# Kernel optimization log

Measured on AMD Instinct MI355X. Metric: run time of the kernel, lower is better.

The kernel has to match this reference:

```python
import jax, jax.numpy as jnp
import numpy as np

N = 100000      # num nodes
E = 1600000     # num edges (avg degree 16)
ND = 32         # node_dim
ED = 32         # edge_dim
OD = 32         # out_dim


def setup_inputs() -> dict:
    key = jax.random.key(0)
    ks = jax.random.split(key, 7)
    node_x = jax.random.normal(ks[0], (N, ND), dtype=jnp.float32)
    edge_x = jax.random.normal(ks[1], (E, ED), dtype=jnp.float32)
    # forward() initializes g.ndata['z'] = torch.rand(N, node_dim+edge_dim)
    z_init = jax.random.uniform(ks[2], (N, ND + ED), dtype=jnp.float32)
    # pre_layer: Linear(ND+ED -> ND+ED); update_layer: Linear(2*ND+ED -> OD)
    W_pre = jax.random.normal(ks[3], (ND + ED, ND + ED), dtype=jnp.float32) / np.sqrt(ND + ED)
    b_pre = jnp.zeros((ND + ED,), dtype=jnp.float32)
    W_upd = jax.random.normal(ks[4], (2 * ND + ED, OD), dtype=jnp.float32) / np.sqrt(2 * ND + ED)
    b_upd = jnp.zeros((OD,), dtype=jnp.float32)
    src = jax.random.randint(ks[5], (E,), 0, N, dtype=jnp.int32)
    dst = jax.random.randint(ks[6], (E,), 0, N, dtype=jnp.int32)
    return {"node_x": node_x, "edge_x": edge_x, "z_init": z_init,
            "W_pre": W_pre, "b_pre": b_pre, "W_upd": W_upd, "b_upd": b_upd,
            "src": src, "dst": dst}


def reference(node_x, edge_x, z_init, W_pre, b_pre, W_upd, b_upd, src, dst):
    n = node_x.shape[0]
    # msg_func: per-edge gather + concat + Linear. Messages depend only on the
    # STATIC node feature 'x', so DGL's topological propagation is equivalent
    # to one edge-parallel pass.
    msg = jnp.concatenate([node_x[src], edge_x], axis=1) @ W_pre + b_pre  # [E, ND+ED]
    # reduce_func: sum over mailbox + ReLU (only fires for nodes with in-edges;
    # nodes with no incoming edges keep the random z_init).
    agg = jax.ops.segment_sum(msg, dst, num_segments=n)                    # [N, ND+ED]
    deg = jax.ops.segment_sum(jnp.ones_like(dst, dtype=node_x.dtype), dst, num_segments=n)
    z = jnp.where((deg > 0)[:, None], jax.nn.relu(agg), z_init)           # [N, ND+ED]
    # node_update: concat + Linear + ReLU
    h = jax.nn.relu(jnp.concatenate([node_x, z], axis=1) @ W_upd + b_upd)  # [N, OD]
    return h
```

## Files before the change

### kernel.cpp

```cpp
#include <hip/hip_runtime.h>


#define N_NODES 100000
#define N_EDGES 1600000
#define ND 32
#define ED 32
#define OD 32
#define ZD 64
#define NTILE 98
#define SLOTS 128
#define NWAVE (N_EDGES / SLOTS + 1)

__device__ inline float bcast(float v, int lane) {
    return __uint_as_float(__builtin_amdgcn_readlane(__float_as_uint(v), lane));
}

__global__ __launch_bounds__(256) void hist8(const int* __restrict__ dst,
                                             int* __restrict__ h8) {
    int e = blockIdx.x * 256 + threadIdx.x;
    if (e < N_EDGES)
        atomicAdd(&h8[(blockIdx.x & 7) * N_NODES + dst[e]], 1);
}

__global__ __launch_bounds__(1024) void scan_part(const int* __restrict__ h8,
                                                  int* __restrict__ cnt,
                                                  int* __restrict__ part) {
    __shared__ int s[1024];
    int i = blockIdx.x * 1024 + threadIdx.x;
    int v = 0;
    if (i < N_NODES) {
        #pragma unroll
        for (int x = 0; x < 8; ++x) v += h8[x * N_NODES + i];
        cnt[i] = v;
    }
    s[threadIdx.x] = v;
    __syncthreads();
    for (int off = 512; off > 0; off >>= 1) {
        if (threadIdx.x < off) s[threadIdx.x] += s[threadIdx.x + off];
        __syncthreads();
    }
    if (threadIdx.x == 0) part[blockIdx.x] = s[0];
}

__global__ void scan_top(int* part) {
    __shared__ int s[128];
    int v = (threadIdx.x < NTILE) ? part[threadIdx.x] : 0;
    s[threadIdx.x] = v;
    __syncthreads();
    for (int off = 1; off < 128; off <<= 1) {
        int u = (threadIdx.x >= off) ? s[threadIdx.x - off] : 0;
        __syncthreads();
        s[threadIdx.x] += u;
        __syncthreads();
    }
    if (threadIdx.x < NTILE) part[threadIdx.x] = s[threadIdx.x] - v;
}

__global__ __launch_bounds__(1024) void scan_local(const int* __restrict__ cnt,
                                                   const int* __restrict__ part,
                                                   const int* __restrict__ h8,
                                                   int* __restrict__ cursor,
                                                   int* __restrict__ c8) {
    __shared__ int s[1024];
    int i = blockIdx.x * 1024 + threadIdx.x;
    int v = (i < N_NODES) ? cnt[i] : 0;
    s[threadIdx.x] = v;
    __syncthreads();
    for (int off = 1; off < 1024; off <<= 1) {
        int u = (threadIdx.x >= off) ? s[threadIdx.x - off] : 0;
        __syncthreads();
        s[threadIdx.x] += u;
        __syncthreads();
    }
    if (i < N_NODES) {
        int run = part[blockIdx.x] + s[threadIdx.x] - v;
        cursor[i] = run;
        #pragma unroll
        for (int x = 0; x < 8; ++x) {
            c8[x * N_NODES + i] = run;
            run += h8[x * N_NODES + i];
        }
    }
}

__global__ __launch_bounds__(256) void permute_ids(
    const int* __restrict__ src, const int* __restrict__ dst,
    int* __restrict__ c8, int2* __restrict__ pair)
{
    int e = blockIdx.x * 256 + threadIdx.x;
    if (e >= N_EDGES) return;
    int pos = atomicAdd(&c8[(blockIdx.x & 7) * N_NODES + dst[e]], 1);
    pair[pos] = make_int2(src[e], e);
}

__device__ inline int lbound(const int* __restrict__ cur, int x) {
    int lo = 0, hi = N_NODES;
    while (lo < hi) {
        int mid = (lo + hi) >> 1;
        if (cur[mid] < x) lo = mid + 1; else hi = mid;
    }
    return lo;
}

__global__ __launch_bounds__(256, 1) void z_csr(
    const float* __restrict__ node_x, const float* __restrict__ edge_x,
    const float* __restrict__ z_init,
    const float* __restrict__ W_pre, const float* __restrict__ b_pre,
    const int* __restrict__ cursor,
    const int2* __restrict__ pair, float* __restrict__ zbuf)
{
    const int l = threadIdx.x & 63;
    float Wp[ZD];
    #pragma unroll
    for (int k = 0; k < ZD; ++k) Wp[k] = W_pre[k * ZD + l];
    const float bp = b_pre[l];
    const float* __restrict__ gbase = (l < ND) ? node_x : (edge_x - ND);

    int w = ((blockIdx.x * 256 + threadIdx.x) >> 6);
    if (w >= NWAVE) return;
    int lo = w * SLOTS;
    int n0 = lbound(cursor, lo);
    int n1 = lbound(cursor, lo + SLOTS);

    for (int n = n0; n < n1; ++n) {
        int j   = cursor[n];
        int end = (n + 1 < N_NODES) ? cursor[n + 1] : N_EDGES;
        int dg  = end - j;
        float z;
        if (dg > 0) {
            float acc = 0.0f;
            for (; j + 8 <= end; j += 8) {
                int2 p0 = pair[j],   p1 = pair[j+1], p2 = pair[j+2], p3 = pair[j+3];
                int2 p4 = pair[j+4], p5 = pair[j+5], p6 = pair[j+6], p7 = pair[j+7];
                int s0 = (l < ND) ? p0.x : p0.y;
                int s1 = (l < ND) ? p1.x : p1.y;
                int s2 = (l < ND) ? p2.x : p2.y;
                int s3 = (l < ND) ? p3.x : p3.y;
                int s4 = (l < ND) ? p4.x : p4.y;
                int s5 = (l < ND) ? p5.x : p5.y;
                int s6 = (l < ND) ? p6.x : p6.y;
                int s7 = (l < ND) ? p7.x : p7.y;
                float v0 = gbase[(unsigned)s0 * 32u + (unsigned)l];
                float v1 = gbase[(unsigned)s1 * 32u + (unsigned)l];
                float v2 = gbase[(unsigned)s2 * 32u + (unsigned)l];
                float v3 = gbase[(unsigned)s3 * 32u + (unsigned)l];
                float v4 = gbase[(unsigned)s4 * 32u + (unsigned)l];
                float v5 = gbase[(unsigned)s5 * 32u + (unsigned)l];
                float v6 = gbase[(unsigned)s6 * 32u + (unsigned)l];
                float v7 = gbase[(unsigned)s7 * 32u + (unsigned)l];
                acc += ((v0 + v1) + (v2 + v3)) + ((v4 + v5) + (v6 + v7));
            }
            for (; j < end; ++j) {
                int2 p0 = pair[j];
                int s0 = (l < ND) ? p0.x : p0.y;
                acc += gbase[(unsigned)s0 * 32u + (unsigned)l];
            }
            float a0 = (float)dg * bp, a1 = 0.0f;
            #pragma unroll
            for (int k = 0; k < ZD; k += 2) {
                a0 += bcast(acc, k)     * Wp[k];
                a1 += bcast(acc, k + 1) * Wp[k + 1];
            }
            z = fmaxf(a0 + a1, 0.0f);
        } else {
            z = z_init[(long)n * ZD + l];
        }
        zbuf[(long)n * ZD + l] = z;
    }
}

__global__ __launch_bounds__(256) void edge_scatter(
    const float* __restrict__ node_x, const float* __restrict__ edge_x,
    const int* __restrict__ src, const int* __restrict__ dst,
    float* __restrict__ S, int* __restrict__ degI)
{
    long t = (long)blockIdx.x * 256 + threadIdx.x;
    int e = (int)(t >> 6), l = (int)(t & 63);
    if (e >= N_EDGES) return;
    int s = src[e], d = dst[e];
    float v = (l < ND) ? node_x[(long)s * ND + l] : edge_x[(long)e * ED + (l - ND)];
    atomicAdd(&S[(long)d * ZD + l], v);
    if (l == 0) atomicAdd(&degI[d], 1);
}

__global__ __launch_bounds__(256, 1) void z_dense(
    const float* __restrict__ z_init,
    const float* __restrict__ W_pre, const float* __restrict__ b_pre,
    float* __restrict__ S, const int* __restrict__ degI)
{
    const int l = threadIdx.x & 63;
    float Wp[ZD];
    #pragma unroll
    for (int k = 0; k < ZD; ++k) Wp[k] = W_pre[k * ZD + l];
    const float bp = b_pre[l];
    int w  = (blockIdx.x * 256 + threadIdx.x) >> 6;
    int nw = (gridDim.x * 256) >> 6;
    for (int n = w; n < N_NODES; n += nw) {
        int dg = degI[n];
        float sv = S[(long)n * ZD + l];
        float z;
        if (dg > 0) {
            float a0 = (float)dg * bp, a1 = 0.0f;
            #pragma unroll
            for (int k = 0; k < ZD; k += 2) {
                a0 += bcast(sv, k)     * Wp[k];
                a1 += bcast(sv, k + 1) * Wp[k + 1];
            }
            z = fmaxf(a0 + a1, 0.0f);
        } else {
            z = z_init[(long)n * ZD + l];
        }
        S[(long)n * ZD + l] = z;
    }
}

__global__ __launch_bounds__(256, 1) void h_upd(
    const float* __restrict__ node_x,
    const float* __restrict__ W_upd, const float* __restrict__ b_upd,
    const float* __restrict__ zbuf, float* __restrict__ out)
{
    const int l = threadIdx.x & 63;
    const int c = l & 31;
    float Wu[ND + ZD];
    #pragma unroll
    for (int k = 0; k < ND + ZD; ++k) Wu[k] = W_upd[k * OD + c];
    const float bu = b_upd[c];
    int w  = (blockIdx.x * 256 + threadIdx.x) >> 6;
    int nw = (gridDim.x * 256) >> 6;
    for (int n = w; n < N_NODES; n += nw) {
        float zv = zbuf[(long)n * ZD + l];
        float xv = node_x[(long)n * ND + c];
        float h0 = bu, h1 = 0.0f;
        #pragma unroll
        for (int k = 0; k < ND; k += 2) {
            h0 += bcast(xv, k)     * Wu[k];
            h1 += bcast(xv, k + 1) * Wu[k + 1];
        }
        #pragma unroll
        for (int k = 0; k < ZD; k += 2) {
            h0 += bcast(zv, k)     * Wu[ND + k];
            h1 += bcast(zv, k + 1) * Wu[ND + k + 1];
        }
        if (l < OD) out[(long)n * OD + l] = fmaxf(h0 + h1, 0.0f);
    }
}

extern "C" void kernel_launch(void* const* d_in, const int* in_sizes, int n_in,
                              void* d_out, int out_size, void* d_ws, size_t ws_size,
                              hipStream_t stream)
{
    const float* node_x = (const float*)d_in[0];
    const float* edge_x = (const float*)d_in[1];
    const float* z_init = (const float*)d_in[2];
    const float* W_pre  = (const float*)d_in[3];
    const float* b_pre  = (const float*)d_in[4];
    const float* W_upd  = (const float*)d_in[5];
    const float* b_upd  = (const float*)d_in[6];
    const int*   src    = (const int*)d_in[7];
    const int*   dst    = (const int*)d_in[8];
    float* out = (float*)d_out;

    size_t need = (size_t)N_EDGES * sizeof(int2)
                + (size_t)N_NODES * ZD * sizeof(float)
                + ((size_t)18 * N_NODES + 128) * sizeof(int);

    if (ws_size >= need) {
        int2*  pair   = (int2*)d_ws;
        float* zbuf   = (float*)(pair + N_EDGES);
        int*   cnt    = (int*)(zbuf + (size_t)N_NODES * ZD);
        int*   part   = cnt + N_NODES;
        int*   cursor = part + 128;
        int*   h8     = cursor + N_NODES;
        int*   c8     = h8 + 8 * N_NODES;

        (void)hipMemsetAsync(h8, 0, 8 * N_NODES * sizeof(int), stream);
        hist8<<<(N_EDGES + 255) / 256, 256, 0, stream>>>(dst, h8);
        scan_part<<<NTILE, 1024, 0, stream>>>(h8, cnt, part);
        scan_top<<<1, 128, 0, stream>>>(part);
        scan_local<<<NTILE, 1024, 0, stream>>>(cnt, part, h8, cursor, c8);
        permute_ids<<<(N_EDGES + 255) / 256, 256, 0, stream>>>(src, dst, c8, pair);
        z_csr<<<(NWAVE * 64 + 255) / 256, 256, 0, stream>>>(
            node_x, edge_x, z_init, W_pre, b_pre, cursor, pair, zbuf);
        h_upd<<<2048, 256, 0, stream>>>(node_x, W_upd, b_upd, zbuf, out);
    } else {
        float* S    = (float*)d_ws;
        int*   degI = (int*)(S + (size_t)N_NODES * ZD);
        (void)hipMemsetAsync(d_ws, 0,
            ((size_t)N_NODES * ZD + N_NODES) * sizeof(float), stream);
        edge_scatter<<<(int)(((long)N_EDGES * 64 + 255) / 256), 256, 0, stream>>>(
            node_x, edge_x, src, dst, S, degI);
        z_dense<<<2048, 256, 0, stream>>>(z_init, W_pre, b_pre, S, degI);
        h_upd<<<2048, 256, 0, stream>>>(node_x, W_upd, b_upd, S, out);
    }
}
```

Baseline: 721.5 us.

## Gather four edges per wave iteration with float4 loads in z_csr

Rewrites the CSR aggregation so each wave handles four edges at once: 16-lane groups each load one edge's 32 node features and 32 edge features as float4, then the groups are reduced with xor shuffles before the readlane-based matvec. Work is also redistributed from equal edge-slot chunks found by binary search to a grid-stride loop of one node per wave, with degree read from cnt. This is meant to cut per-edge load instructions and latency chains, but tail edges are handled with clamped masked loads, and load balance now depends on node degree.

```diff
diff --git a/kernel.cpp b/kernel.cpp
--- a/kernel.cpp
+++ b/kernel.cpp
@@ -8,8 +8,6 @@
 #define OD 32
 #define ZD 64
 #define NTILE 98
-#define SLOTS 128
-#define NWAVE (N_EDGES / SLOTS + 1)
 
 __device__ inline float bcast(float v, int lane) {
     return __uint_as_float(__builtin_amdgcn_readlane(__float_as_uint(v), lane));
@@ -93,73 +91,67 @@
     pair[pos] = make_int2(src[e], e);
 }
 
-__device__ inline int lbound(const int* __restrict__ cur, int x) {
-    int lo = 0, hi = N_NODES;
-    while (lo < hi) {
-        int mid = (lo + hi) >> 1;
-        if (cur[mid] < x) lo = mid + 1; else hi = mid;
-    }
-    return lo;
-}
-
 __global__ __launch_bounds__(256, 1) void z_csr(
     const float* __restrict__ node_x, const float* __restrict__ edge_x,
     const float* __restrict__ z_init,
     const float* __restrict__ W_pre, const float* __restrict__ b_pre,
-    const int* __restrict__ cursor,
+    const int* __restrict__ cnt, const int* __restrict__ cursor,
     const int2* __restrict__ pair, float* __restrict__ zbuf)
 {
     const int l = threadIdx.x & 63;
+    const int c = l & 7;
+    const int h = (l >> 3) & 1;
+    const int s = l >> 4;
+    const float4* __restrict__ b4 =
+        h ? (const float4*)edge_x : (const float4*)node_x;
+
     float Wp[ZD];
     #pragma unroll
     for (int k = 0; k < ZD; ++k) Wp[k] = W_pre[k * ZD + l];
     const float bp = b_pre[l];
-    const float* __restrict__ gbase = (l < ND) ? node_x : (edge_x - ND);
-
-    int w = ((blockIdx.x * 256 + threadIdx.x) >> 6);
-    if (w >= NWAVE) return;
-    int lo = w * SLOTS;
-    int n0 = lbound(cursor, lo);
-    int n1 = lbound(cursor, lo + SLOTS);
-
-    for (int n = n0; n < n1; ++n) {
-        int j   = cursor[n];
-        int end = (n + 1 < N_NODES) ? cursor[n + 1] : N_EDGES;
-        int dg  = end - j;
+
+    int w  = (blockIdx.x * 256 + threadIdx.x) >> 6;
+    int nw = (gridDim.x * 256) >> 6;
+    for (int n = w; n < N_NODES; n += nw) {
+        int dg = cnt[n];
         float z;
         if (dg > 0) {
-            float acc = 0.0f;
-            for (; j + 8 <= end; j += 8) {
-                int2 p0 = pair[j],   p1 = pair[j+1], p2 = pair[j+2], p3 = pair[j+3];
-                int2 p4 = pair[j+4], p5 = pair[j+5], p6 = pair[j+6], p7 = pair[j+7];
-                int s0 = (l < ND) ? p0.x : p0.y;
-                int s1 = (l < ND) ? p1.x : p1.y;
-                int s2 = (l < ND) ? p2.x : p2.y;
-                int s3 = (l < ND) ? p3.x : p3.y;
-                int s4 = (l < ND) ? p4.x : p4.y;
-                int s5 = (l < ND) ? p5.x : p5.y;
-                int s6 = (l < ND) ? p6.x : p6.y;
-                int s7 = (l < ND) ? p7.x : p7.y;
-                float v0 = gbase[(unsigned)s0 * 32u + (unsigned)l];
-                float v1 = gbase[(unsigned)s1 * 32u + (unsigned)l];
-                float v2 = gbase[(unsigned)s2 * 32u + (unsigned)l];
-                float v3 = gbase[(unsigned)s3 * 32u + (unsigned)l];
-                float v4 = gbase[(unsigned)s4 * 32u + (unsigned)l];
-                float v5 = gbase[(unsigned)s5 * 32u + (unsigned)l];
-                float v6 = gbase[(unsigned)s6 * 32u + (unsigned)l];
-                float v7 = gbase[(unsigned)s7 * 32u + (unsigned)l];
-                acc += ((v0 + v1) + (v2 + v3)) + ((v4 + v5) + (v6 + v7));
+            int j0  = cursor[n];
+            int end = j0 + dg;
+            float4 acc = make_float4(0.f, 0.f, 0.f, 0.f);
+            for (int j = j0; j < end; j += 16) {
+                #pragma unroll
+                for (int u = 0; u < 4; ++u) {
+                    int ei   = j + 4 * u + s;
+                    int cl   = (ei < end) ? ei : (end - 1);
+                    int2 q   = pair[cl];
+                    int row  = h ? q.y : q.x;
+                    float4 v = b4[(unsigned)row * 8u + (unsigned)c];
+                    float  m = (ei < end) ? 1.0f : 0.0f;
+                    acc.x += v.x * m;
+                    acc.y += v.y * m;
+                    acc.z += v.z * m;
+                    acc.w += v.w * m;
+                }
             }
-            for (; j < end; ++j) {
-                int2 p0 = pair[j];
-                int s0 = (l < ND) ? p0.x : p0.y;
-                acc += gbase[(unsigned)s0 * 32u + (unsigned)l];
-            }
+            acc.x += __shfl_xor(acc.x, 16); acc.y += __shfl_xor(acc.y, 16);
+            acc.z += __shfl_xor(acc.z, 16); acc.w += __shfl_xor(acc.w, 16);
+            acc.x += __shfl_xor(acc.x, 32); acc.y += __shfl_xor(acc.y, 32);
+            acc.z += __shfl_xor(acc.z, 32); acc.w += __shfl_xor(acc.w, 32);
             float a0 = (float)dg * bp, a1 = 0.0f;
             #pragma unroll
             for (int k = 0; k < ZD; k += 2) {
-                a0 += bcast(acc, k)     * Wp[k];
-                a1 += bcast(acc, k + 1) * Wp[k + 1];
+                const int sl0 = (k >> 5) * 8 + ((k & 31) >> 2);
+                const float cv0 = ((k & 3) == 0) ? acc.x :
+                                  ((k & 3) == 1) ? acc.y :
+                                  ((k & 3) == 2) ? acc.z : acc.w;
+                const int k1 = k + 1;
+                const int sl1 = (k1 >> 5) * 8 + ((k1 & 31) >> 2);
+                const float cv1 = ((k1 & 3) == 0) ? acc.x :
+                                  ((k1 & 3) == 1) ? acc.y :
+                                  ((k1 & 3) == 2) ? acc.z : acc.w;
+                a0 += bcast(cv0, sl0) * Wp[k];
+                a1 += bcast(cv1, sl1) * Wp[k1];
             }
             z = fmaxf(a0 + a1, 0.0f);
         } else {
@@ -279,8 +271,8 @@
         scan_top<<<1, 128, 0, stream>>>(part);
         scan_local<<<NTILE, 1024, 0, stream>>>(cnt, part, h8, cursor, c8);
         permute_ids<<<(N_EDGES + 255) / 256, 256, 0, stream>>>(src, dst, c8, pair);
-        z_csr<<<(NWAVE * 64 + 255) / 256, 256, 0, stream>>>(
-            node_x, edge_x, z_init, W_pre, b_pre, cursor, pair, zbuf);
+        z_csr<<<2048, 256, 0, stream>>>(node_x, edge_x, z_init, W_pre, b_pre,
+                                        cnt, cursor, pair, zbuf);
         h_upd<<<2048, 256, 0, stream>>>(node_x, W_upd, b_upd, zbuf, out);
     } else {
         float* S    = (float*)d_ws;
```

Result: faster. 589.5 us (-18.3%).
